# Performance work log

Measured on AMD Instinct MI355X. Metric: run time of the kernel, lower is better.

The kernel has to match this reference:

```python
import jax, jax.numpy as jnp
import numpy as np

B, S, A, M, H, OUT = 256, 256, 256, 256, 8, 256
KD = A // H   # key_dim per head = 32
VD = M // H   # value_dim per head = 32


def setup_inputs() -> dict:
    key = jax.random.key(0)
    ks = jax.random.split(key, 11)
    return {
        "q_data": jax.random.normal(ks[0], (B, S, A), dtype=jnp.float32),
        "m_data": jax.random.normal(ks[1], (B, S, M), dtype=jnp.float32),
        "bias": jax.random.normal(ks[2], (B, 1, 1, S), dtype=jnp.float32),
        "nonbatched_bias": jax.random.normal(ks[3], (H, S, S), dtype=jnp.float32),
        "query_w": jax.random.normal(ks[4], (A, H, KD), dtype=jnp.float32) * 0.05,
        "key_w": jax.random.normal(ks[5], (M, H, KD), dtype=jnp.float32) * 0.05,
        "value_w": jax.random.normal(ks[6], (M, H, VD), dtype=jnp.float32) * 0.05,
        "gating_w": jax.random.normal(ks[7], (A, H, VD), dtype=jnp.float32) * 0.05,
        "gating_b": jax.random.normal(ks[8], (H, VD), dtype=jnp.float32) * 0.05,
        "output_w": jax.random.normal(ks[9], (H, VD, OUT), dtype=jnp.float32) * 0.05,
        "output_b": jax.random.normal(ks[10], (OUT,), dtype=jnp.float32) * 0.05,
    }


def reference(q_data, m_data, bias, nonbatched_bias,
              query_w, key_w, value_w, gating_w, gating_b, output_w, output_b):
    key_dim = query_w.shape[-1]
    # projections
    q = jnp.einsum('bqa,ahc->bqhc', q_data, query_w) * key_dim ** (-0.5)
    k = jnp.einsum('bka,ahc->bkhc', m_data, key_w)
    v = jnp.einsum('bka,ahc->bkhc', m_data, value_w)
    # logits [b,h,q,k] with batched + shared bias
    logits = jnp.einsum('bqhc,bkhc->bhqk', q, k) + bias + nonbatched_bias[None]
    weights = jax.nn.softmax(logits, axis=-1)
    weighted_avg = jnp.einsum('bhqk,bkhc->bqhc', weights, v)
    # sigmoid gating
    gate_values = jax.nn.sigmoid(jnp.einsum('bqc,chv->bqhv', q_data, gating_w) + gating_b)
    weighted_avg = weighted_avg * gate_values
    # output projection
    output = jnp.einsum('bqhc,hco->bqo', weighted_avg, output_w) + output_b
    return output
```

## Files before the change

### kernel.cpp

```cpp
#include <hip/hip_runtime.h>

typedef unsigned short u16;
typedef __attribute__((ext_vector_type(8))) short short8;
typedef __attribute__((ext_vector_type(4))) float f32x4;
typedef __attribute__((ext_vector_type(4))) unsigned int u32x4;
typedef __attribute__((ext_vector_type(4))) unsigned short u16x4;

#define LOG2E 1.4426950408889634f

__device__ __forceinline__ float bf2f(u16 u) {
    union { float f; unsigned int i; } c; c.i = ((unsigned int)u) << 16; return c.f;
}
__device__ __forceinline__ u16 f2bf(float f) {
    unsigned int x = __float_as_uint(f);
    x += 0x7fff + ((x >> 16) & 1);
    return (u16)(x >> 16);
}

union Cvt32 { u32x4 v[4]; u16 u[32]; };

__device__ __forceinline__ void ld32f_bf(const float* __restrict__ p, Cvt32& t) {
#pragma unroll
    for (int j = 0; j < 32; j += 4) {
        f32x4 x = *(const f32x4*)(p + j);
        t.u[j]     = f2bf(x[0]);
        t.u[j + 1] = f2bf(x[1]);
        t.u[j + 2] = f2bf(x[2]);
        t.u[j + 3] = f2bf(x[3]);
    }
}


__global__ __launch_bounds__(256) void prep_a(
    const float* __restrict__ q_data, const float* __restrict__ m_data,
    const float* __restrict__ qw, const float* __restrict__ kw,
    const float* __restrict__ vw, const float* __restrict__ gw,
    const float* __restrict__ ow,
    u16* __restrict__ qbf, u16* __restrict__ mbf,
    u16* __restrict__ wt, u16* __restrict__ WoT)
{
    int blk = blockIdx.x, tid = threadIdx.x;
    if (blk < 32768) {
        const float* src = (blk < 16384) ? q_data : m_data;
        u16* dst = (blk < 16384) ? qbf : mbf;
        int i = (blk & 16383) * 1024 + tid * 4;
        f32x4 x = *(const f32x4*)(src + i);
        u16x4 o = { f2bf(x[0]), f2bf(x[1]), f2bf(x[2]), f2bf(x[3]) };
        *(u16x4*)(dst + i) = o;
    } else if (blk < 33792) {
        int e = (blk - 32768) * 256 + tid;
        int n = e & 255, k = (e >> 8) & 255, g = e >> 16;
        const float* W = g == 0 ? kw : g == 1 ? vw : g == 2 ? qw : gw;
        wt[(((g << 8) | n) << 8) | k] = f2bf(W[k * 256 + n]);
    } else {
        int e = (blk - 33792) * 256 + tid;
        int o = e & 255, hc = e >> 8;
        WoT[o * 256 + hc] = f2bf(ow[hc * 256 + o]);
    }
}

__global__ __launch_bounds__(256) void prep_nbT(
    const float* __restrict__ nb, u16* __restrict__ nbT)
{
    __shared__ float tile[64][65];
    int q0 = blockIdx.x * 64, k0 = blockIdx.y * 64, h = blockIdx.z;
    int tid = threadIdx.x;
    int rr = tid >> 4;
    int cc = (tid & 15) << 2;
    const float* src = nb + ((size_t)(h * 256 + q0)) * 256 + k0;
#pragma unroll
    for (int p = 0; p < 4; p++) {
        int q = rr + p * 16;
        f32x4 x = *(const f32x4*)(src + (size_t)q * 256 + cc);
        tile[q][cc] = x[0]; tile[q][cc + 1] = x[1];
        tile[q][cc + 2] = x[2]; tile[q][cc + 3] = x[3];
    }
    __syncthreads();
    u16* dst = nbT + ((size_t)(h * 256 + k0)) * 256 + q0;
#pragma unroll
    for (int p = 0; p < 4; p++) {
        int k = rr + p * 16;
        u16x4 o;
#pragma unroll
        for (int u = 0; u < 4; u++) o[u] = f2bf(tile[cc + u][k] * LOG2E);
        *(u16x4*)(dst + (size_t)k * 256 + cc) = o;
    }
}

__global__ __launch_bounds__(256) void proj_a(
    const u16* __restrict__ mbf, const u16* __restrict__ qbf,
    const u16* __restrict__ wt,
    u16* __restrict__ Kh, u16* __restrict__ Vh, u16* __restrict__ Qh,
    u16* __restrict__ GW, const float* __restrict__ gb)
{
    __shared__ u16 As[128 * 40];
    __shared__ u16 Bs[128 * 40];
    int tid = threadIdx.x;
    int lane = tid & 63, w = tid >> 6;
    int wm = w >> 1, wn = w & 1;
    int row0 = blockIdx.x * 128;
    int n0 = blockIdx.y * 128;
    int g = blockIdx.y >> 1;
    const u16* X = (g < 2) ? mbf : qbf;
    int lr = tid >> 1;
    int lc = (tid & 1) << 4;

    const f32x4 fz = {0.f, 0.f, 0.f, 0.f};
    f32x4 acc[4][4];
#pragma unroll
    for (int i = 0; i < 4; i++)
#pragma unroll
        for (int j = 0; j < 4; j++) acc[i][j] = fz;

    int kl = (lane >> 4) << 3;
    int l15 = lane & 15;
    int rm = wm * 64 + l15;
    int rn = wn * 64 + l15;

    for (int kb = 0; kb < 8; ++kb) {
        int k0 = kb << 5;
        const u16* pa = X + ((size_t)(row0 + lr) << 8) + k0 + lc;
        u32x4 a0 = *(const u32x4*)pa;
        u32x4 a1 = *(const u32x4*)(pa + 8);
        const u16* pb = wt + ((size_t)(n0 + lr) << 8) + k0 + lc;
        u32x4 b0 = *(const u32x4*)pb;
        u32x4 b1 = *(const u32x4*)(pb + 8);
        if (kb) __syncthreads();
        *(u32x4*)&As[lr * 40 + lc] = a0;
        *(u32x4*)&As[lr * 40 + lc + 8] = a1;
        *(u32x4*)&Bs[lr * 40 + lc] = b0;
        *(u32x4*)&Bs[lr * 40 + lc + 8] = b1;
        __syncthreads();
        short8 af[4], bf[4];
#pragma unroll
        for (int i = 0; i < 4; i++) af[i] = *(const short8*)&As[(rm + i * 16) * 40 + kl];
#pragma unroll
        for (int i = 0; i < 4; i++) bf[i] = *(const short8*)&Bs[(rn + i * 16) * 40 + kl];
#pragma unroll
        for (int mi = 0; mi < 4; mi++)
#pragma unroll
            for (int ni = 0; ni < 4; ni++)
                acc[mi][ni] = __builtin_amdgcn_mfma_f32_16x16x32_bf16(af[mi], bf[ni], acc[mi][ni], 0, 0, 0);
    }

    u16* dst = (g == 0) ? Kh : (g == 1) ? Vh : (g == 2) ? Qh : GW;
    float scale = (g == 2) ? 0.17677669529663687f * LOG2E : 1.f;
#pragma unroll
    for (int mi = 0; mi < 4; mi++)
#pragma unroll
        for (int ni = 0; ni < 4; ni++)
#pragma unroll
            for (int r = 0; r < 4; r++) {
                int row = row0 + wm * 64 + mi * 16 + ((lane >> 4) << 2) + r;
                int col = n0 + wn * 64 + ni * 16 + l15;
                float v = acc[mi][ni][r] * scale;
                int hc = col & 255;
                if (g == 3) v = (v + gb[hc]) * LOG2E;
                int b = row >> 8, s = row & 255, h = hc >> 5, c = col & 31;
                dst[((((size_t)b * 8 + h) << 8) + s) * 32 + c] = f2bf(v);
            }
}

__global__ __launch_bounds__(256, 3) void attn_a(
    const u16* __restrict__ Qh, const u16* __restrict__ Kh,
    const u16* __restrict__ Vh, u16* GW,
    const float* __restrict__ bias2, const u16* __restrict__ nbT)
{
    __shared__ u16 smem[25344];
    u16* Vt = smem;
    int bid = blockIdx.x;
    int b = bid >> 3, h = bid & 7;
    int tid = threadIdx.x, lane = tid & 63, w = tid >> 6;
    int l15 = lane & 15;
    int kl = (lane >> 4) << 3;
    int rq = (lane >> 4) << 2;
    size_t hoff = ((size_t)(b * 8 + h)) << 13;
    const f32x4 fz = {0.f, 0.f, 0.f, 0.f};
    u16* myP = smem + 8448 + w * 4224;

    {
        const u16* p = Vh + hoff + (tid << 5);
        Cvt32 tm;
        tm.v[0] = *(const u32x4*)p;        tm.v[1] = *(const u32x4*)(p + 8);
        tm.v[2] = *(const u32x4*)(p + 16); tm.v[3] = *(const u32x4*)(p + 24);
#pragma unroll
        for (int c = 0; c < 32; c++) Vt[c * 264 + tid] = tm.u[c];
    }
    float bload[16];
#pragma unroll
    for (int t = 0; t < 16; t++)
        bload[t] = bias2[(b << 8) + t * 16 + l15] * LOG2E;
    short8 kf[16];
#pragma unroll
    for (int t = 0; t < 16; t++)
        kf[t] = *(const short8*)(Kh + hoff + (size_t)(t * 16 + l15) * 32 + kl);
    __syncthreads();

    const u16* nbh = nbT + ((size_t)h << 16);

#pragma unroll 1
    for (int mt = 0; mt < 4; ++mt) {
        int q0 = 64 * w + mt * 16 + rq;
        short8 qf = *(const short8*)(Qh + hoff + (size_t)(64 * w + mt * 16 + l15) * 32 + kl);

        u16 gv[8];
#pragma unroll
        for (int ni = 0; ni < 2; ++ni)
#pragma unroll
            for (int r = 0; r < 4; r++)
                gv[ni * 4 + r] = GW[hoff + (size_t)(q0 + r) * 32 + ni * 16 + l15];

        const u16* nbp = nbh + q0;
        float srow[4] = {0.f, 0.f, 0.f, 0.f};
#pragma unroll
        for (int hf = 0; hf < 2; ++hf) {
            f32x4 sc[8];
#pragma unroll
            for (int t = 0; t < 8; t++) {
                int tt = hf * 8 + t;
                f32x4 cb = {bload[tt], bload[tt], bload[tt], bload[tt]};
                sc[t] = __builtin_amdgcn_mfma_f32_16x16x32_bf16(qf, kf[tt], cb, 0, 0, 0);
            }
#pragma unroll
            for (int t = 0; t < 8; t++) {
                int tt = hf * 8 + t;
                u16x4 nbv = *(const u16x4*)(nbp + ((tt * 16 + l15) << 8));
#pragma unroll
                for (int r = 0; r < 4; r++) {
                    float p = __builtin_amdgcn_exp2f(sc[t][r] + bf2f(nbv[r]));
                    srow[r] += p;
                    myP[(rq + r) * 264 + tt * 16 + l15] = f2bf(p);
                }
            }
        }
#pragma unroll
        for (int r = 0; r < 4; r++) {
            float s = srow[r];
            s += __shfl_xor(s, 1);
            s += __shfl_xor(s, 2);
            s += __shfl_xor(s, 4);
            s += __shfl_xor(s, 8);
            srow[r] = __builtin_amdgcn_rcpf(s);
        }

        f32x4 oacc[2] = {fz, fz};
#pragma unroll
        for (int ks = 0; ks < 8; ++ks) {
            short8 pf = *(const short8*)&myP[l15 * 264 + ks * 32 + kl];
#pragma unroll
            for (int ni = 0; ni < 2; ++ni) {
                short8 vf = *(const short8*)&Vt[(ni * 16 + l15) * 264 + ks * 32 + kl];
                oacc[ni] = __builtin_amdgcn_mfma_f32_16x16x32_bf16(pf, vf, oacc[ni], 0, 0, 0);
            }
        }

#pragma unroll
        for (int ni = 0; ni < 2; ++ni)
#pragma unroll
            for (int r = 0; r < 4; r++) {
                float gate = __builtin_amdgcn_rcpf(1.f + __builtin_amdgcn_exp2f(-bf2f(gv[ni * 4 + r])));
                size_t idx = hoff + (size_t)(q0 + r) * 32 + ni * 16 + l15;
                GW[idx] = f2bf(oacc[ni][r] * srow[r] * gate);
            }
    }
}

__global__ __launch_bounds__(256) void gemmout_a(
    const u16* __restrict__ WA, const u16* __restrict__ WoT,
    float* __restrict__ dst, const float* __restrict__ ob)
{
    __shared__ u16 As[128 * 40];
    __shared__ u16 Bs[128 * 40];
    int tid = threadIdx.x;
    int lane = tid & 63, w = tid >> 6;
    int wm = w >> 1, wn = w & 1;
    int row0 = blockIdx.x * 128;
    int n0 = blockIdx.y * 128;
    int bq = row0 >> 8, s0 = row0 & 255;
    int lr = tid >> 1;
    int lc = (tid & 1) << 4;

    const f32x4 fz = {0.f, 0.f, 0.f, 0.f};
    f32x4 acc[4][4];
#pragma unroll
    for (int i = 0; i < 4; i++)
#pragma unroll
        for (int j = 0; j < 4; j++) acc[i][j] = fz;

    int kl = (lane >> 4) << 3;
    int l15 = lane & 15;
    int rm = wm * 64 + l15;
    int rn = wn * 64 + l15;

    for (int kb = 0; kb < 8; ++kb) {
        int k0 = kb << 5;
        const u16* pa = WA + ((((size_t)bq * 8 + kb) << 8) + s0 + lr) * 32 + lc;
        u32x4 a0 = *(const u32x4*)pa;
        u32x4 a1 = *(const u32x4*)(pa + 8);
        const u16* pb = WoT + ((size_t)(n0 + lr) << 8) + k0 + lc;
        u32x4 b0 = *(const u32x4*)pb;
        u32x4 b1 = *(const u32x4*)(pb + 8);
        if (kb) __syncthreads();
        *(u32x4*)&As[lr * 40 + lc] = a0;
        *(u32x4*)&As[lr * 40 + lc + 8] = a1;
        *(u32x4*)&Bs[lr * 40 + lc] = b0;
        *(u32x4*)&Bs[lr * 40 + lc + 8] = b1;
        __syncthreads();
        short8 af[4], bf[4];
#pragma unroll
        for (int i = 0; i < 4; i++) af[i] = *(const short8*)&As[(rm + i * 16) * 40 + kl];
#pragma unroll
        for (int i = 0; i < 4; i++) bf[i] = *(const short8*)&Bs[(rn + i * 16) * 40 + kl];
#pragma unroll
        for (int mi = 0; mi < 4; mi++)
#pragma unroll
            for (int ni = 0; ni < 4; ni++)
                acc[mi][ni] = __builtin_amdgcn_mfma_f32_16x16x32_bf16(af[mi], bf[ni], acc[mi][ni], 0, 0, 0);
    }

#pragma unroll
    for (int mi = 0; mi < 4; mi++)
#pragma unroll
        for (int ni = 0; ni < 4; ni++)
#pragma unroll
            for (int r = 0; r < 4; r++) {
                int row = row0 + wm * 64 + mi * 16 + ((lane >> 4) << 2) + r;
                int col = n0 + wn * 64 + ni * 16 + l15;
                dst[((size_t)row << 8) + col] = acc[mi][ni][r] + ob[col];
            }
}


__global__ __launch_bounds__(256) void transpose_k(
    const float* __restrict__ query_w, const float* __restrict__ key_w,
    const float* __restrict__ value_w, const float* __restrict__ gating_w,
    u16* __restrict__ wt)
{
    int i = blockIdx.x * 256 + threadIdx.x;
    int half = i >> 17;
    int rem = i & 131071;
    int h = rem >> 14, e = rem & 16383;
    int n = e >> 8, k = e & 255;
    int src_idx = k * 256 + h * 32 + (n & 31);
    float v;
    if (half == 0) v = (n < 32) ? key_w[src_idx]   : value_w[src_idx];
    else           v = (n < 32) ? query_w[src_idx] : gating_w[src_idx];
    wt[i] = f2bf(v);
}

__global__ __launch_bounds__(256) void fused_attn_k(
    const float* __restrict__ q_data, const float* __restrict__ m_data,
    const float* __restrict__ bias2, const float* __restrict__ nb,
    const u16* __restrict__ wt, const float* __restrict__ gb,
    u16* __restrict__ WAo)
{
    __shared__ u16 smem[31488];
    u16* Ksh = smem;
    u16* Vt  = smem + 10240;
    u16* Xs  = smem + 18688;
    u16* Wsh = smem + 28928;

    int bid = blockIdx.x;
    int b = bid >> 3, h = bid & 7;
    int tid = threadIdx.x, lane = tid & 63, w = tid >> 6;
    int l15 = lane & 15;
    int kl = (lane >> 4) << 3;
    int rq = (lane >> 4) << 2;
    const f32x4 fz = {0.f, 0.f, 0.f, 0.f};

    float bload[16];
#pragma unroll
    for (int t = 0; t < 16; t++) bload[t] = bias2[(b << 8) + t * 16 + l15];
    float gbc0 = gb[h * 32 + l15];
    float gbc1 = gb[h * 32 + 16 + l15];

    const float* Xg = m_data + ((size_t)b << 16);
    const u16* Wg = wt + (h << 14);
    f32x4 acc[4][4];
#pragma unroll
    for (int i = 0; i < 4; i++)
#pragma unroll
        for (int j = 0; j < 4; j++) acc[i][j] = fz;

    for (int kb = 0; kb < 8; ++kb) {
        Cvt32 am;
        ld32f_bf(Xg + (size_t)tid * 256 + kb * 32, am);
        u32x4 b0, b1;
        int nrow = tid >> 1, nc = (tid & 1) << 4;
        if (tid < 128) {
            const u16* q = Wg + nrow * 256 + kb * 32 + nc;
            b0 = *(const u32x4*)q; b1 = *(const u32x4*)(q + 8);
        }
        if (kb) __syncthreads();
        *(u32x4*)&Xs[tid * 40]      = am.v[0];
        *(u32x4*)&Xs[tid * 40 + 8]  = am.v[1];
        *(u32x4*)&Xs[tid * 40 + 16] = am.v[2];
        *(u32x4*)&Xs[tid * 40 + 24] = am.v[3];
        if (tid < 128) {
            *(u32x4*)&Wsh[nrow * 40 + nc] = b0;
            *(u32x4*)&Wsh[nrow * 40 + nc + 8] = b1;
        }
        __syncthreads();
        short8 af[4], bf[4];
#pragma unroll
        for (int i = 0; i < 4; i++) af[i] = *(const short8*)&Xs[(64 * w + i * 16 + l15) * 40 + kl];
#pragma unroll
        for (int i = 0; i < 4; i++) bf[i] = *(const short8*)&Wsh[(i * 16 + l15) * 40 + kl];
#pragma unroll
        for (int mi = 0; mi < 4; mi++)
#pragma unroll
            for (int ni = 0; ni < 4; ni++)
                acc[mi][ni] = __builtin_amdgcn_mfma_f32_16x16x32_bf16(af[mi], bf[ni], acc[mi][ni], 0, 0, 0);
    }
#pragma unroll
    for (int mi = 0; mi < 4; mi++)
#pragma unroll
        for (int ni = 0; ni < 4; ni++)
#pragma unroll
            for (int r = 0; r < 4; r++) {
                int s = 64 * w + mi * 16 + rq + r;
                int col = ni * 16 + l15;
                u16 v = f2bf(acc[mi][ni][r]);
                if (ni < 2) Ksh[s * 40 + col] = v;
                else        Vt[(col - 32) * 264 + s] = v;
            }
    __syncthreads();

    const float* Xg2 = q_data + ((size_t)b << 16);
    const u16* Wg2 = wt + 131072 + (h << 14);
    f32x4 acc2[4][4];
#pragma unroll
    for (int i = 0; i < 4; i++)
#pragma unroll
        for (int j = 0; j < 4; j++) acc2[i][j] = fz;

    for (int kb = 0; kb < 8; ++kb) {
        Cvt32 am;
        ld32f_bf(Xg2 + (size_t)tid * 256 + kb * 32, am);
        u32x4 b0, b1;
        int nrow = tid >> 1, nc = (tid & 1) << 4;
        if (tid < 128) {
            const u16* q = Wg2 + nrow * 256 + kb * 32 + nc;
            b0 = *(const u32x4*)q; b1 = *(const u32x4*)(q + 8);
        }
        __syncthreads();
        *(u32x4*)&Xs[tid * 40]      = am.v[0];
        *(u32x4*)&Xs[tid * 40 + 8]  = am.v[1];
        *(u32x4*)&Xs[tid * 40 + 16] = am.v[2];
        *(u32x4*)&Xs[tid * 40 + 24] = am.v[3];
        if (tid < 128) {
            *(u32x4*)&Wsh[nrow * 40 + nc] = b0;
            *(u32x4*)&Wsh[nrow * 40 + nc + 8] = b1;
        }
        __syncthreads();
        short8 af[4], bf[4];
#pragma unroll
        for (int i = 0; i < 4; i++) af[i] = *(const short8*)&Xs[(64 * w + i * 16 + l15) * 40 + kl];
#pragma unroll
        for (int i = 0; i < 4; i++) bf[i] = *(const short8*)&Wsh[(i * 16 + l15) * 40 + kl];
#pragma unroll
        for (int mi = 0; mi < 4; mi++)
#pragma unroll
            for (int ni = 0; ni < 4; ni++)
                acc2[mi][ni] = __builtin_amdgcn_mfma_f32_16x16x32_bf16(af[mi], bf[ni], acc2[mi][ni], 0, 0, 0);
    }
    __syncthreads();

    u16* myQ = smem + 18688 + w * 2816;
    u16* myP = myQ + 640;
    const float* nbp = nb + ((size_t)h << 16);
    const float qscale = 0.17677669529663687f;

#pragma unroll 1
    for (int mt = 0; mt < 4; ++mt) {
#pragma unroll
        for (int ni = 0; ni < 2; ++ni)
#pragma unroll
            for (int r = 0; r < 4; r++)
                myQ[(rq + r) * 40 + ni * 16 + l15] = f2bf(acc2[mt][ni][r] * qscale);

        short8 qf = *(const short8*)&myQ[l15 * 40 + kl];
        f32x4 sc[16];
#pragma unroll
        for (int t = 0; t < 16; t++) {
            short8 kfr = *(const short8*)&Ksh[(t * 16 + l15) * 40 + kl];
            sc[t] = __builtin_amdgcn_mfma_f32_16x16x32_bf16(qf, kfr, fz, 0, 0, 0);
        }

        int q0 = 64 * w + mt * 16 + rq;
        float mrow[4] = {-3e30f, -3e30f, -3e30f, -3e30f};
#pragma unroll
        for (int t = 0; t < 16; t++) {
            int kidx = t * 16 + l15;
#pragma unroll
            for (int r = 0; r < 4; r++) {
                float v = sc[t][r] + bload[t] + nbp[(size_t)(q0 + r) * 256 + kidx];
                sc[t][r] = v;
                mrow[r] = fmaxf(mrow[r], v);
            }
        }
#pragma unroll
        for (int r = 0; r < 4; r++) {
            float m = mrow[r];
            m = fmaxf(m, __shfl_xor(m, 1));
            m = fmaxf(m, __shfl_xor(m, 2));
            m = fmaxf(m, __shfl_xor(m, 4));
            m = fmaxf(m, __shfl_xor(m, 8));
            mrow[r] = m;
        }
        float srow[4] = {0.f, 0.f, 0.f, 0.f};
#pragma unroll
        for (int t = 0; t < 16; t++)
#pragma unroll
            for (int r = 0; r < 4; r++) {
                float p = __expf(sc[t][r] - mrow[r]);
                sc[t][r] = p;
                srow[r] += p;
            }
#pragma unroll
        for (int r = 0; r < 4; r++) {
            float s = srow[r];
            s += __shfl_xor(s, 1);
            s += __shfl_xor(s, 2);
            s += __shfl_xor(s, 4);
            s += __shfl_xor(s, 8);
            srow[r] = 1.f / s;
        }

        f32x4 oacc[2] = {fz, fz};
#pragma unroll
        for (int half = 0; half < 2; ++half) {
#pragma unroll
            for (int t = 0; t < 8; t++)
#pragma unroll
                for (int r = 0; r < 4; r++)
                    myP[(rq + r) * 136 + t * 16 + l15] =
                        f2bf(sc[half * 8 + t][r] * srow[r]);
#pragma unroll
            for (int ks = 0; ks < 4; ++ks) {
                short8 pf = *(const short8*)&myP[l15 * 136 + ks * 32 + kl];
#pragma unroll
                for (int ni = 0; ni < 2; ++ni) {
                    short8 vf = *(const short8*)&Vt[(ni * 16 + l15) * 264 + half * 128 + ks * 32 + kl];
                    oacc[ni] = __builtin_amdgcn_mfma_f32_16x16x32_bf16(pf, vf, oacc[ni], 0, 0, 0);
                }
            }
        }

#pragma unroll
        for (int ni = 0; ni < 2; ++ni) {
            float gbv = ni ? gbc1 : gbc0;
#pragma unroll
            for (int r = 0; r < 4; r++) {
                float gate = 1.f / (1.f + __expf(-(acc2[mt][ni + 2][r] + gbv)));
                size_t idx = (((size_t)b << 8) + q0 + r) * 256 + h * 32 + ni * 16 + l15;
                WAo[idx] = f2bf(oacc[ni][r] * gate);
            }
        }
    }
}

__global__ __launch_bounds__(256) void gemm_out_k(
    const u16* __restrict__ X, const float* __restrict__ Wo,
    float* __restrict__ dst, const float* __restrict__ cbias)
{
    __shared__ u16 As[128 * 40];
    __shared__ u16 Bs[128 * 40];
    int tid = threadIdx.x;
    int lane = tid & 63, w = tid >> 6;
    int wm = w >> 1, wn = w & 1;
    int row0 = blockIdx.x * 128;
    int n0 = blockIdx.y * 128;
    int lr = tid >> 1;
    int lc = (tid & 1) << 4;

    const f32x4 fz = {0.f, 0.f, 0.f, 0.f};
    f32x4 acc[4][4];
#pragma unroll
    for (int i = 0; i < 4; i++)
#pragma unroll
        for (int j = 0; j < 4; j++) acc[i][j] = fz;

    int kl = (lane >> 4) << 3;
    int l15 = lane & 15;
    int rm = wm * 64 + l15;
    int rn = wn * 64 + l15;

    for (int kb = 0; kb < 8; ++kb) {
        int k0 = kb << 5;
        const u16* pa = X + ((size_t)(row0 + lr) << 8) + k0 + lc;
        u32x4 a0 = *(const u32x4*)pa;
        u32x4 a1 = *(const u32x4*)(pa + 8);
        int bk = tid >> 3, bn = (tid & 7) << 4;
        const float* pb = Wo + (size_t)(k0 + bk) * 256 + n0 + bn;
        u16 bu[16];
#pragma unroll
        for (int j = 0; j < 16; j += 4) {
            f32x4 x = *(const f32x4*)(pb + j);
            bu[j] = f2bf(x[0]); bu[j + 1] = f2bf(x[1]);
            bu[j + 2] = f2bf(x[2]); bu[j + 3] = f2bf(x[3]);
        }
        if (kb) __syncthreads();
        *(u32x4*)&As[lr * 40 + lc] = a0;
        *(u32x4*)&As[lr * 40 + lc + 8] = a1;
#pragma unroll
        for (int j = 0; j < 16; j++) Bs[(bn + j) * 40 + bk] = bu[j];
        __syncthreads();
        short8 af[4], bf[4];
#pragma unroll
        for (int i = 0; i < 4; i++) af[i] = *(const short8*)&As[(rm + i * 16) * 40 + kl];
#pragma unroll
        for (int i = 0; i < 4; i++) bf[i] = *(const short8*)&Bs[(rn + i * 16) * 40 + kl];
#pragma unroll
        for (int mi = 0; mi < 4; mi++)
#pragma unroll
            for (int ni = 0; ni < 4; ni++)
                acc[mi][ni] = __builtin_amdgcn_mfma_f32_16x16x32_bf16(af[mi], bf[ni], acc[mi][ni], 0, 0, 0);
    }

#pragma unroll
    for (int mi = 0; mi < 4; mi++)
#pragma unroll
        for (int ni = 0; ni < 4; ni++)
#pragma unroll
            for (int r = 0; r < 4; r++) {
                int row = row0 + wm * 64 + mi * 16 + ((lane >> 4) << 2) + r;
                int col = n0 + wn * 64 + ni * 16 + l15;
                dst[((size_t)row << 8) + col] = acc[mi][ni][r] + cbias[col];
            }
}

extern "C" void kernel_launch(void* const* d_in, const int* in_sizes, int n_in,
                              void* d_out, int out_size, void* d_ws, size_t ws_size,
                              hipStream_t stream)
{
    const float* q_data   = (const float*)d_in[0];
    const float* m_data   = (const float*)d_in[1];
    const float* bias     = (const float*)d_in[2];
    const float* nb       = (const float*)d_in[3];
    const float* query_w  = (const float*)d_in[4];
    const float* key_w    = (const float*)d_in[5];
    const float* value_w  = (const float*)d_in[6];
    const float* gating_w = (const float*)d_in[7];
    const float* gating_b = (const float*)d_in[8];
    const float* output_w = (const float*)d_in[9];
    const float* output_b = (const float*)d_in[10];

    const size_t NEED_A = 4ull * 33554432 + 524288 + 131072 + 1048576;

    if (ws_size >= NEED_A) {
        u16* ws   = (u16*)d_ws;
        u16* Kh   = ws;
        u16* Vh   = Kh + 16777216;
        u16* Qh   = Vh + 16777216;
        u16* GW   = Qh + 16777216;
        u16* wt   = GW + 16777216;
        u16* WoT  = wt + 262144;
        u16* nbT  = WoT + 65536;
        u16* qbf  = (u16*)d_out;
        u16* mbf  = qbf + 16777216;

        prep_a<<<34048, 256, 0, stream>>>(q_data, m_data,
                                          query_w, key_w, value_w, gating_w, output_w,
                                          qbf, mbf, wt, WoT);
        prep_nbT<<<dim3(4, 4, 8), 256, 0, stream>>>(nb, nbT);
        proj_a<<<dim3(512, 8), 256, 0, stream>>>(mbf, qbf, wt, Kh, Vh, Qh, GW, gating_b);
        attn_a<<<2048, 256, 0, stream>>>(Qh, Kh, Vh, GW, bias, nbT);
        gemmout_a<<<dim3(512, 2), 256, 0, stream>>>(GW, WoT, (float*)d_out, output_b);
    } else {
        u16* WAb = (u16*)d_ws;
        u16* wt  = (u16*)d_out;
        transpose_k<<<1024, 256, 0, stream>>>(query_w, key_w, value_w, gating_w, wt);
        fused_attn_k<<<2048, 256, 0, stream>>>(q_data, m_data, bias, nb, wt, gating_b, WAb);
        gemm_out_k<<<dim3(512, 2), 256, 0, stream>>>(WAb, output_w, (float*)d_out, output_b);
    }
}
```

Before: 424.4 us.

## Fuse input bf16 conversion into projection GEMM and streamline attention P·V

```diff
diff --git a/kernel.cpp b/kernel.cpp
--- a/kernel.cpp
+++ b/kernel.cpp
@@ -32,76 +32,70 @@
 
 
 __global__ __launch_bounds__(256) void prep_a(
-    const float* __restrict__ q_data, const float* __restrict__ m_data,
+    const float* __restrict__ nb,
     const float* __restrict__ qw, const float* __restrict__ kw,
     const float* __restrict__ vw, const float* __restrict__ gw,
     const float* __restrict__ ow,
-    u16* __restrict__ qbf, u16* __restrict__ mbf,
-    u16* __restrict__ wt, u16* __restrict__ WoT)
-{
+    u16* __restrict__ wt, u16* __restrict__ WoT, u16* __restrict__ nbT)
+{
+    __shared__ float tile[64][65];
     int blk = blockIdx.x, tid = threadIdx.x;
-    if (blk < 32768) {
-        const float* src = (blk < 16384) ? q_data : m_data;
-        u16* dst = (blk < 16384) ? qbf : mbf;
-        int i = (blk & 16383) * 1024 + tid * 4;
-        f32x4 x = *(const f32x4*)(src + i);
-        u16x4 o = { f2bf(x[0]), f2bf(x[1]), f2bf(x[2]), f2bf(x[3]) };
-        *(u16x4*)(dst + i) = o;
-    } else if (blk < 33792) {
-        int e = (blk - 32768) * 256 + tid;
+    if (blk < 1024) {
+        int e = blk * 256 + tid;
         int n = e & 255, k = (e >> 8) & 255, g = e >> 16;
         const float* W = g == 0 ? kw : g == 1 ? vw : g == 2 ? qw : gw;
         wt[(((g << 8) | n) << 8) | k] = f2bf(W[k * 256 + n]);
-    } else {
-        int e = (blk - 33792) * 256 + tid;
+    } else if (blk < 1280) {
+        int e = (blk - 1024) * 256 + tid;
         int o = e & 255, hc = e >> 8;
         WoT[o * 256 + hc] = f2bf(ow[hc * 256 + o]);
-    }
-}
-
-__global__ __launch_bounds__(256) void prep_nbT(
-    const float* __restrict__ nb, u16* __restrict__ nbT)
-{
-    __shared__ float tile[64][65];
-    int q0 = blockIdx.x * 64, k0 = blockIdx.y * 64, h = blockIdx.z;
-    int tid = threadIdx.x;
-    int rr = tid >> 4;
-    int cc = (tid & 15) << 2;
-    const float* src = nb + ((size_t)(h * 256 + q0)) * 256 + k0;
-#pragma unroll
-    for (int p = 0; p < 4; p++) {
-        int q = rr + p * 16;
-        f32x4 x = *(const f32x4*)(src + (size_t)q * 256 + cc);
-        tile[q][cc] = x[0]; tile[q][cc + 1] = x[1];
-        tile[q][cc + 2] = x[2]; tile[q][cc + 3] = x[3];
-    }
-    __syncthreads();
-    u16* dst = nbT + ((size_t)(h * 256 + k0)) * 256 + q0;
-#pragma unroll
-    for (int p = 0; p < 4; p++) {
-        int k = rr + p * 16;
-        u16x4 o;
-#pragma unroll
-        for (int u = 0; u < 4; u++) o[u] = f2bf(tile[cc + u][k] * LOG2E);
-        *(u16x4*)(dst + (size_t)k * 256 + cc) = o;
+    } else {
+        int idx = blk - 1280;
+        int q0 = (idx & 3) * 64, k0 = ((idx >> 2) & 3) * 64, h = idx >> 4;
+        int rr = tid >> 4;
+        int cc = (tid & 15) << 2;
+        const float* src = nb + ((size_t)(h * 256 + q0)) * 256 + k0;
+#pragma unroll
+        for (int p = 0; p < 4; p++) {
+            int q = rr + p * 16;
+            f32x4 x = *(const f32x4*)(src + (size_t)q * 256 + cc);
+            tile[q][cc] = x[0]; tile[q][cc + 1] = x[1];
+            tile[q][cc + 2] = x[2]; tile[q][cc + 3] = x[3];
+        }
+        __syncthreads();
+        u16* dst = nbT + ((size_t)(h * 256 + k0)) * 256 + q0;
+#pragma unroll
+        for (int p = 0; p < 4; p++) {
+            int k = rr + p * 16;
+            u16x4 o;
+#pragma unroll
+            for (int u = 0; u < 4; u++) o[u] = f2bf(tile[cc + u][k] * LOG2E);
+            *(u16x4*)(dst + (size_t)k * 256 + cc) = o;
+        }
     }
 }
 
 __global__ __launch_bounds__(256) void proj_a(
-    const u16* __restrict__ mbf, const u16* __restrict__ qbf,
+    const float* __restrict__ m_data, const float* __restrict__ q_data,
     const u16* __restrict__ wt,
     u16* __restrict__ Kh, u16* __restrict__ Vh, u16* __restrict__ Qh,
     u16* __restrict__ GW, const float* __restrict__ gb)
 {
     __shared__ u16 As[128 * 40];
     __shared__ u16 Bs[128 * 40];
+    int bid = blockIdx.x;
+    int xcd = bid & 7;
+    int slot = bid >> 3;
+    int y = slot & 7;
+    int x = ((slot >> 3) << 3) | xcd;
+    int row0 = x * 128;
+    int n0 = y * 128;
+    int g = y >> 1;
+    const float* X = (g < 2) ? m_data : q_data;
+
     int tid = threadIdx.x;
     int lane = tid & 63, w = tid >> 6;
     int wm = w >> 1, wn = w & 1;
-    int row0 = blockIdx.x * 128;
-    int n0 = blockIdx.y * 128;
-    int g = blockIdx.y >> 1;
-    const u16* X = (g < 2) ? mbf : qbf;
     int lr = tid >> 1;
     int lc = (tid & 1) << 4;
 
@@ -119,15 +113,22 @@
 
     for (int kb = 0; kb < 8; ++kb) {
         int k0 = kb << 5;
-        const u16* pa = X + ((size_t)(row0 + lr) << 8) + k0 + lc;
-        u32x4 a0 = *(const u32x4*)pa;
-        u32x4 a1 = *(const u32x4*)(pa + 8);
+        const float* pa = X + (size_t)(row0 + lr) * 256 + k0 + lc;
+        f32x4 x0 = *(const f32x4*)pa;
+        f32x4 x1 = *(const f32x4*)(pa + 4);
+        f32x4 x2 = *(const f32x4*)(pa + 8);
+        f32x4 x3 = *(const f32x4*)(pa + 12);
+        union { u32x4 v[2]; u16 u[16]; } am;
+        am.u[0] = f2bf(x0[0]); am.u[1] = f2bf(x0[1]); am.u[2] = f2bf(x0[2]); am.u[3] = f2bf(x0[3]);
+        am.u[4] = f2bf(x1[0]); am.u[5] = f2bf(x1[1]); am.u[6] = f2bf(x1[2]); am.u[7] = f2bf(x1[3]);
+        am.u[8] = f2bf(x2[0]); am.u[9] = f2bf(x2[1]); am.u[10] = f2bf(x2[2]); am.u[11] = f2bf(x2[3]);
+        am.u[12] = f2bf(x3[0]); am.u[13] = f2bf(x3[1]); am.u[14] = f2bf(x3[2]); am.u[15] = f2bf(x3[3]);
         const u16* pb = wt + ((size_t)(n0 + lr) << 8) + k0 + lc;
         u32x4 b0 = *(const u32x4*)pb;
         u32x4 b1 = *(const u32x4*)(pb + 8);
         if (kb) __syncthreads();
-        *(u32x4*)&As[lr * 40 + lc] = a0;
-        *(u32x4*)&As[lr * 40 + lc + 8] = a1;
+        *(u32x4*)&As[lr * 40 + lc] = am.v[0];
+        *(u32x4*)&As[lr * 40 + lc + 8] = am.v[1];
         *(u32x4*)&Bs[lr * 40 + lc] = b0;
         *(u32x4*)&Bs[lr * 40 + lc + 8] = b1;
         __syncthreads();
@@ -161,12 +162,12 @@
             }
 }
 
-__global__ __launch_bounds__(256, 3) void attn_a(
+__global__ __launch_bounds__(256, 4) void attn_a(
     const u16* __restrict__ Qh, const u16* __restrict__ Kh,
     const u16* __restrict__ Vh, u16* GW,
     const float* __restrict__ bias2, const u16* __restrict__ nbT)
 {
-    __shared__ u16 smem[25344];
+    __shared__ u16 smem[17152];
     u16* Vt = smem;
     int bid = blockIdx.x;
     int b = bid >> 3, h = bid & 7;
@@ -176,7 +177,7 @@
     int rq = (lane >> 4) << 2;
     size_t hoff = ((size_t)(b * 8 + h)) << 13;
     const f32x4 fz = {0.f, 0.f, 0.f, 0.f};
-    u16* myP = smem + 8448 + w * 4224;
+    u16* myP = smem + 8448 + w * 2176;
 
     {
         const u16* p = Vh + hoff + (tid << 5);
@@ -212,6 +213,7 @@
 
         const u16* nbp = nbh + q0;
         float srow[4] = {0.f, 0.f, 0.f, 0.f};
+        f32x4 oacc[2] = {fz, fz};
 #pragma unroll
         for (int hf = 0; hf < 2; ++hf) {
             f32x4 sc[8];
@@ -229,7 +231,19 @@
                 for (int r = 0; r < 4; r++) {
                     float p = __builtin_amdgcn_exp2f(sc[t][r] + bf2f(nbv[r]));
                     srow[r] += p;
-                    myP[(rq + r) * 264 + tt * 16 + l15] = f2bf(p);
+                    int row = rq + r;
+                    int pidx = (row * 136 + t * 16 + l15) ^ ((row & 8) << 1);
+                    myP[pidx] = f2bf(p);
+                }
+            }
+#pragma unroll
+            for (int ks = 0; ks < 4; ++ks) {
+                int ridx = (l15 * 136 + ks * 32 + kl) ^ ((l15 & 8) << 1);
+                short8 pf = *(const short8*)&myP[ridx];
+#pragma unroll
+                for (int ni = 0; ni < 2; ++ni) {
+                    short8 vf = *(const short8*)&Vt[(ni * 16 + l15) * 264 + hf * 128 + ks * 32 + kl];
+                    oacc[ni] = __builtin_amdgcn_mfma_f32_16x16x32_bf16(pf, vf, oacc[ni], 0, 0, 0);
                 }
             }
         }
@@ -243,25 +257,19 @@
             srow[r] = __builtin_amdgcn_rcpf(s);
         }
 
-        f32x4 oacc[2] = {fz, fz};
-#pragma unroll
-        for (int ks = 0; ks < 8; ++ks) {
-            short8 pf = *(const short8*)&myP[l15 * 264 + ks * 32 + kl];
-#pragma unroll
-            for (int ni = 0; ni < 2; ++ni) {
-                short8 vf = *(const short8*)&Vt[(ni * 16 + l15) * 264 + ks * 32 + kl];
-                oacc[ni] = __builtin_amdgcn_mfma_f32_16x16x32_bf16(pf, vf, oacc[ni], 0, 0, 0);
-            }
-        }
-
 #pragma unroll
         for (int ni = 0; ni < 2; ++ni)
 #pragma unroll
             for (int r = 0; r < 4; r++) {
                 float gate = __builtin_amdgcn_rcpf(1.f + __builtin_amdgcn_exp2f(-bf2f(gv[ni * 4 + r])));
-                size_t idx = hoff + (size_t)(q0 + r) * 32 + ni * 16 + l15;
-                GW[idx] = f2bf(oacc[ni][r] * srow[r] * gate);
-            }
+                int row = rq + r;
+                int oidx = (row * 40 + ni * 16 + l15) ^ ((row & 8) << 1);
+                myP[oidx] = f2bf(oacc[ni][r] * srow[r] * gate);
+            }
+        int orow = lane >> 2, ocol = (lane & 3) << 3;
+        int ridx = (orow * 40 + ocol) ^ ((orow & 8) << 1);
+        u32x4 ov = *(const u32x4*)&myP[ridx];
+        *(u32x4*)(GW + hoff + (size_t)(64 * w + mt * 16 + orow) * 32 + ocol) = ov;
     }
 }
 
@@ -657,14 +665,10 @@
         u16* wt   = GW + 16777216;
         u16* WoT  = wt + 262144;
         u16* nbT  = WoT + 65536;
-        u16* qbf  = (u16*)d_out;
-        u16* mbf  = qbf + 16777216;
-
-        prep_a<<<34048, 256, 0, stream>>>(q_data, m_data,
-                                          query_w, key_w, value_w, gating_w, output_w,
-                                          qbf, mbf, wt, WoT);
-        prep_nbT<<<dim3(4, 4, 8), 256, 0, stream>>>(nb, nbT);
-        proj_a<<<dim3(512, 8), 256, 0, stream>>>(mbf, qbf, wt, Kh, Vh, Qh, GW, gating_b);
+
+        prep_a<<<1408, 256, 0, stream>>>(nb, query_w, key_w, value_w, gating_w,
+                                         output_w, wt, WoT, nbT);
+        proj_a<<<4096, 256, 0, stream>>>(m_data, q_data, wt, Kh, Vh, Qh, GW, gating_b);
         attn_a<<<2048, 256, 0, stream>>>(Qh, Kh, Vh, GW, bias, nbT);
         gemmout_a<<<dim3(512, 2), 256, 0, stream>>>(GW, WoT, (float*)d_out, output_b);
     } else {
```

Measured after the change: 556.5 us. 31.1% more time.
